# Performance work log

Hardware: AMD Instinct MI355X
Metric: run time of the kernel (lower is better)

The kernel has to match this reference:

```python
import jax, jax.numpy as jnp
import numpy as np

N = 50000      # nodes
E = 800000     # edges (avg degree 16)
IN = 128       # in_channels
OUT = 200      # out_channels


def setup_inputs() -> dict:
    key = jax.random.key(0)
    ks = jax.random.split(key, 12)
    x = jax.random.normal(ks[0], (N, IN), dtype=jnp.float32)
    src = jax.random.randint(ks[1], (E,), 0, N, dtype=jnp.int32)
    off = jax.random.randint(ks[2], (E,), 1, N, dtype=jnp.int32)
    dst = (src + off) % N  # guarantees no self-loops (PyG ChebConv removes them)
    edge_index = jnp.stack([src, dst])
    edge_weight = jax.random.uniform(ks[3], (E,), dtype=jnp.float32) + 0.1
    s = 0.05
    # scale_1 (K=1): one weight; scale_2 (K=2): two; scale_3 (K=3): three. Biases per scale.
    return {
        "x": x,
        "edge_index": edge_index,
        "edge_weight": edge_weight,
        "w1_0": jax.random.normal(ks[4], (IN, OUT), dtype=jnp.float32) * s,
        "b1": jnp.zeros((OUT,), dtype=jnp.float32),
        "w2_0": jax.random.normal(ks[5], (IN, OUT), dtype=jnp.float32) * s,
        "w2_1": jax.random.normal(ks[6], (IN, OUT), dtype=jnp.float32) * s,
        "b2": jnp.zeros((OUT,), dtype=jnp.float32),
        "w3_0": jax.random.normal(ks[7], (IN, OUT), dtype=jnp.float32) * s,
        "w3_1": jax.random.normal(ks[8], (IN, OUT), dtype=jnp.float32) * s,
        "w3_2": jax.random.normal(ks[9], (IN, OUT), dtype=jnp.float32) * s,
        "b3": jnp.zeros((OUT,), dtype=jnp.float32),
    }


def _cheb_norm(edge_index, edge_weight, num_nodes):
    # PyG ChebConv.__norm__ with normalization='sym', lambda_max=2.0:
    # L = I - D^{-1/2} A D^{-1/2}; Lhat = 2L/lambda_max - I = -D^{-1/2} A D^{-1/2}
    # (self-loop weights become exactly 0, so we can drop them)
    row, col = edge_index[0], edge_index[1]
    deg = jax.ops.segment_sum(edge_weight, row, num_segments=num_nodes)
    dis = jnp.where(deg > 0, jax.lax.rsqrt(deg), 0.0)
    return -dis[row] * edge_weight * dis[col]


def _propagate(h, src, dst, norm, num_nodes):
    # out[i] = sum_{(j->i) in E} norm_e * h[j]
    return jax.ops.segment_sum(norm[:, None] * h[src], dst, num_segments=num_nodes)


def reference(x, edge_index, edge_weight, w1_0, b1, w2_0, w2_1, b2, w3_0, w3_1, w3_2, b3):
    num_nodes = x.shape[0]
    src, dst = edge_index[0], edge_index[1]
    norm = _cheb_norm(edge_index, edge_weight, num_nodes)
    # Chebyshev recursion (shared across the three scales; identical math):
    tx0 = x                                              # T_0(L) x
    tx1 = _propagate(tx0, src, dst, norm, num_nodes)     # T_1(L) x = Lhat x
    tx2 = 2.0 * _propagate(tx1, src, dst, norm, num_nodes) - tx0  # T_2(L) x
    s1 = tx0 @ w1_0 + b1
    s2 = tx0 @ w2_0 + tx1 @ w2_1 + b2
    s3 = tx0 @ w3_0 + tx1 @ w3_1 + tx2 @ w3_2 + b3
    return (s1, s2, s3)
```

## Files before the change

kernel.cpp:

```cpp
#include <hip/hip_runtime.h>

#define IN 128
#define OUT 200
#define NT 13
#define MT 64

typedef __bf16 bf16x8 __attribute__((ext_vector_type(8)));
typedef float f32x4 __attribute__((ext_vector_type(4)));
typedef unsigned short ushort;
typedef ushort ushort8 __attribute__((ext_vector_type(8)));
typedef unsigned int uint;

__device__ inline ushort f2bf(float f) {
  uint b = __float_as_uint(f);
  return (ushort)((b + 0x7FFFu + ((b >> 16) & 1u)) >> 16);
}
__device__ inline float bf_lo(uint v) { return __uint_as_float(v << 16); }
__device__ inline float bf_hi(uint v) { return __uint_as_float(v & 0xFFFF0000u); }

__device__ inline size_t pk_idx(int row, int ch) {
  int rt = row >> 4, lr = row & 15, kk = ch >> 5, hi = (ch & 31) >> 3;
  return ((size_t)(rt * 4 + kk) * 64 + hi * 16 + lr) * 8 + (ch & 7);
}

__device__ inline void gload16(const void* g, void* l) {
  __builtin_amdgcn_global_load_lds(
      (const __attribute__((address_space(1))) void*)g,
      (__attribute__((address_space(3))) void*)l, 16, 0, 0);
}


__global__ void k_deg_cnt(const int* __restrict__ src, const int* __restrict__ dst,
                          const float* __restrict__ w, float* __restrict__ deg8,
                          int* __restrict__ cnt8, int E, int N) {
  int e = blockIdx.x * blockDim.x + threadIdx.x;
  if (e >= E) return;
  int copy = blockIdx.x & 7;
  atomicAdd(&deg8[(size_t)copy * N + src[e]], w[e]);
  atomicAdd(&cnt8[(size_t)copy * N + dst[e]], 1);
}

__global__ void k_dis_scan(const float* __restrict__ deg8, const int* __restrict__ cnt8,
                           float* __restrict__ dis, int* __restrict__ pref8,
                           int* __restrict__ offs, int* __restrict__ bsum, int n) {
  __shared__ int s[256];
  int t = threadIdx.x;
  int i = blockIdx.x * 256 + t;
  int v = 0;
  if (i < n) {
    float d = 0.f;
    int run = 0;
#pragma unroll
    for (int c = 0; c < 8; ++c) {
      pref8[(size_t)c * n + i] = run;
      run += cnt8[(size_t)c * n + i];
      d += deg8[(size_t)c * n + i];
    }
    v = run;
    dis[i] = d > 0.f ? rsqrtf(d) : 0.f;
  }
  s[t] = v;
  __syncthreads();
  for (int o = 1; o < 256; o <<= 1) {
    int a = (t >= o) ? s[t - o] : 0;
    __syncthreads();
    s[t] += a;
    __syncthreads();
  }
  if (i < n) offs[i] = s[t] - v;
  if (t == 255) bsum[blockIdx.x] = s[255];
}

__global__ void k_scan_c2(int* __restrict__ offs, const int* __restrict__ bsum,
                          int n, int E) {
  __shared__ int red[256];
  int t = threadIdx.x;
  int partial = 0;
  for (int i = t; i < (int)blockIdx.x; i += 256) partial += bsum[i];
  red[t] = partial;
  __syncthreads();
  for (int o = 128; o > 0; o >>= 1) {
    if (t < o) red[t] += red[t + o];
    __syncthreads();
  }
  int base = red[0];
  int i = blockIdx.x * 256 + t;
  if (i < n) offs[i] += base;
  if (i == 0) offs[n] = E;
}

__global__ void k_fill(const int* __restrict__ src, const int* __restrict__ dst,
                       const float* __restrict__ w, const float* __restrict__ dis,
                       const int* __restrict__ offs, const int* __restrict__ pref8,
                       int* __restrict__ cursor8, int2* __restrict__ csr_rec,
                       int E, int N) {
  int e = blockIdx.x * blockDim.x + threadIdx.x;
  if (e >= E) return;
  int copy = blockIdx.x & 7;
  int sN = src[e], d = dst[e];
  int pos = offs[d] + pref8[(size_t)copy * N + d]
          + atomicAdd(&cursor8[(size_t)copy * N + d], 1);
  float nm = -dis[sN] * w[e] * dis[d];
  csr_rec[pos] = make_int2(sN, __float_as_int(nm));
}


__global__ void k_cast_pack(const float* __restrict__ x, ushort* __restrict__ xb,
                            ushort* __restrict__ xp, int cast_blocks, long totx,
                            const float* __restrict__ w10, const float* __restrict__ w20,
                            const float* __restrict__ w21, const float* __restrict__ w30,
                            const float* __restrict__ w31, const float* __restrict__ w32,
                            ushort* __restrict__ wpack) {
  if (blockIdx.x < (unsigned)cast_blocks) {
    long i = ((long)blockIdx.x * blockDim.x + threadIdx.x) * 8;
    if (i >= totx) return;
    float4 a = *(const float4*)&x[i];
    float4 b = *(const float4*)&x[i + 4];
    ushort8 o;
    o[0] = f2bf(a.x); o[1] = f2bf(a.y); o[2] = f2bf(a.z); o[3] = f2bf(a.w);
    o[4] = f2bf(b.x); o[5] = f2bf(b.y); o[6] = f2bf(b.z); o[7] = f2bf(b.w);
    *(ushort8*)&xb[i] = o;
    int row = (int)(i >> 7), ch = (int)(i & 127);
    *(ushort8*)&xp[pk_idx(row, ch)] = o;
  } else {
    int gid = (blockIdx.x - cast_blocks) * blockDim.x + threadIdx.x;
    int total = 6 * NT * 4 * 64;
    if (gid >= total) return;
    int lane = gid & 63;
    int f = gid >> 6;
    int kk = f & 3;
    int g2 = f >> 2;
    int m = g2 % 6;
    int t = g2 / 6;
    const float* w = (m == 0) ? w10 : (m == 1) ? w20 : (m == 2) ? w21
                   : (m == 3) ? w30 : (m == 4) ? w31 : w32;
    int col = t * 16 + (lane & 15);
    int kbase = kk * 32 + (lane >> 4) * 8;
    ushort8 o;
#pragma unroll
    for (int j = 0; j < 8; ++j)
      o[j] = (col < OUT) ? f2bf(w[(kbase + j) * OUT + col]) : (ushort)0;
    *(ushort8*)&wpack[(size_t)gid * 8] = o;
  }
}


template <int MODE>
__global__ void k_gather(const ushort* __restrict__ h, const ushort* __restrict__ xb,
                         const int2* __restrict__ csr_rec,
                         const int* __restrict__ offs, ushort* __restrict__ out_lin,
                         ushort* __restrict__ out_pk, int n) {
  int node = blockIdx.x * 4 + (threadIdx.x >> 6);
  if (node >= n) return;
  int lane = threadIdx.x & 63;
  int ch0 = lane * 2;
  int s = offs[node], e = offs[node + 1];
  float lo[8], hi[8];
#pragma unroll
  for (int q = 0; q < 8; ++q) { lo[q] = 0.f; hi[q] = 0.f; }
  int p = s;
  for (; p + 7 < e; p += 8) {
    int2 rec[8]; uint v[8];
#pragma unroll
    for (int q = 0; q < 8; ++q) rec[q] = csr_rec[p + q];
#pragma unroll
    for (int q = 0; q < 8; ++q) v[q] = *(const uint*)&h[(size_t)rec[q].x * IN + ch0];
#pragma unroll
    for (int q = 0; q < 8; ++q) {
      float nm = __int_as_float(rec[q].y);
      lo[q] = fmaf(nm, bf_lo(v[q]), lo[q]);
      hi[q] = fmaf(nm, bf_hi(v[q]), hi[q]);
    }
  }
  for (; p + 1 < e; p += 2) {
    int2 r0 = csr_rec[p], r1 = csr_rec[p + 1];
    uint v0 = *(const uint*)&h[(size_t)r0.x * IN + ch0];
    uint v1 = *(const uint*)&h[(size_t)r1.x * IN + ch0];
    float n0 = __int_as_float(r0.y), n1 = __int_as_float(r1.y);
    lo[0] = fmaf(n0, bf_lo(v0), lo[0]); hi[0] = fmaf(n0, bf_hi(v0), hi[0]);
    lo[1] = fmaf(n1, bf_lo(v1), lo[1]); hi[1] = fmaf(n1, bf_hi(v1), hi[1]);
  }
  if (p < e) {
    int2 r0 = csr_rec[p];
    float n0 = __int_as_float(r0.y);
    uint v0 = *(const uint*)&h[(size_t)r0.x * IN + ch0];
    lo[2] = fmaf(n0, bf_lo(v0), lo[2]); hi[2] = fmaf(n0, bf_hi(v0), hi[2]);
  }
  float r0 = ((lo[0] + lo[1]) + (lo[2] + lo[3])) + ((lo[4] + lo[5]) + (lo[6] + lo[7]));
  float r1 = ((hi[0] + hi[1]) + (hi[2] + hi[3])) + ((hi[4] + hi[5]) + (hi[6] + hi[7]));
  if (MODE == 1) {
    uint xv = *(const uint*)&xb[(size_t)node * IN + ch0];
    r0 = 2.f * r0 - bf_lo(xv);
    r1 = 2.f * r1 - bf_hi(xv);
  }
  uint packed = (uint)f2bf(r0) | ((uint)f2bf(r1) << 16);
  if (MODE == 0)
    *(uint*)&out_lin[(size_t)node * IN + ch0] = packed;
  *(uint*)&out_pk[pk_idx(node, ch0)] = packed;
}


__global__ __launch_bounds__(256) void k_gemm_mfma(
    const ushort* __restrict__ xp, const ushort* __restrict__ t1p, const ushort* __restrict__ t2p,
    const ushort* __restrict__ wpack,
    const float* __restrict__ b1v, const float* __restrict__ b2v, const float* __restrict__ b3v,
    float* __restrict__ out, int n) {
  __shared__ ushort bsm[2][24 * 512];
  int lane = threadIdx.x & 63;
  int wave = threadIdx.x >> 6;
  int row0 = blockIdx.x * MT + wave * 16;
  int rt = row0 >> 4;

  bf16x8 a[3][4];
  const ushort* mats[3] = {xp, t1p, t2p};
#pragma unroll
  for (int m = 0; m < 3; ++m) {
#pragma unroll
    for (int kk = 0; kk < 4; ++kk) {
      size_t fi = ((size_t)rt * 4 + kk) * 512 + (size_t)lane * 8;
      a[m][kk] = __builtin_bit_cast(bf16x8, *(const ushort8*)&mats[m][fi]);
    }
  }
#pragma unroll
  for (int m = 0; m < 3; ++m)
#pragma unroll
    for (int kk = 0; kk < 4; ++kk)
      asm volatile("" : "+v"(a[m][kk]));

  long NS = (long)n * OUT;
  float* out1 = out;
  float* out2 = out + NS;
  float* out3 = out + 2 * NS;

  auto stage = [&](int t, int buf) {
    const ushort* src = wpack + (size_t)t * 24 * 512;
#pragma unroll
    for (int j = 0; j < 6; ++j) {
      int c = wave * 6 + j;
      gload16(src + (size_t)c * 512 + (size_t)lane * 8, &bsm[buf][c * 512]);
    }
  };

  stage(0, 0);
  __syncthreads();
  int cur = 0;

  for (int t = 0; t < NT; ++t) {
    if (t + 1 < NT) stage(t + 1, cur ^ 1);

    int col = t * 16 + (lane & 15);
    bool colok = col < OUT;
    int colc = colok ? col : 0;
    float bb1 = colok ? b1v[colc] : 0.f;
    float bb2 = colok ? b2v[colc] : 0.f;
    float bb3 = colok ? b3v[colc] : 0.f;
    f32x4 c1 = {bb1, bb1, bb1, bb1};
    f32x4 c2 = {bb2, bb2, bb2, bb2};
    f32x4 c3 = {bb3, bb3, bb3, bb3};

    const ushort* bb = &bsm[cur][0];
#pragma unroll
    for (int kk = 0; kk < 4; ++kk) {
      bf16x8 b10 = __builtin_bit_cast(bf16x8, *(const ushort8*)&bb[(0 * 4 + kk) * 512 + lane * 8]);
      bf16x8 b20 = __builtin_bit_cast(bf16x8, *(const ushort8*)&bb[(1 * 4 + kk) * 512 + lane * 8]);
      bf16x8 b21 = __builtin_bit_cast(bf16x8, *(const ushort8*)&bb[(2 * 4 + kk) * 512 + lane * 8]);
      bf16x8 b30 = __builtin_bit_cast(bf16x8, *(const ushort8*)&bb[(3 * 4 + kk) * 512 + lane * 8]);
      bf16x8 b31 = __builtin_bit_cast(bf16x8, *(const ushort8*)&bb[(4 * 4 + kk) * 512 + lane * 8]);
      bf16x8 b32 = __builtin_bit_cast(bf16x8, *(const ushort8*)&bb[(5 * 4 + kk) * 512 + lane * 8]);
      c1 = __builtin_amdgcn_mfma_f32_16x16x32_bf16(a[0][kk], b10, c1, 0, 0, 0);
      c2 = __builtin_amdgcn_mfma_f32_16x16x32_bf16(a[0][kk], b20, c2, 0, 0, 0);
      c2 = __builtin_amdgcn_mfma_f32_16x16x32_bf16(a[1][kk], b21, c2, 0, 0, 0);
      c3 = __builtin_amdgcn_mfma_f32_16x16x32_bf16(a[0][kk], b30, c3, 0, 0, 0);
      c3 = __builtin_amdgcn_mfma_f32_16x16x32_bf16(a[1][kk], b31, c3, 0, 0, 0);
      c3 = __builtin_amdgcn_mfma_f32_16x16x32_bf16(a[2][kk], b32, c3, 0, 0, 0);
    }

    if (colok) {
      int rbase = row0 + (lane >> 4) * 4;
#pragma unroll
      for (int r = 0; r < 4; ++r) {
        int ra = rbase + r;
        if (ra < n) {
          out1[(long)ra * OUT + col] = c1[r];
          out2[(long)ra * OUT + col] = c2[r];
          out3[(long)ra * OUT + col] = c3[r];
        }
      }
    }

    __syncthreads();
    cur ^= 1;
  }
}


extern "C" void kernel_launch(void* const* d_in, const int* in_sizes, int n_in,
                              void* d_out, int out_size, void* d_ws, size_t ws_size,
                              hipStream_t stream) {
  const float* x   = (const float*)d_in[0];
  const int*   ei  = (const int*)d_in[1];
  const float* ew  = (const float*)d_in[2];
  const float* w10 = (const float*)d_in[3];
  const float* b1  = (const float*)d_in[4];
  const float* w20 = (const float*)d_in[5];
  const float* w21 = (const float*)d_in[6];
  const float* b2  = (const float*)d_in[7];
  const float* w30 = (const float*)d_in[8];
  const float* w31 = (const float*)d_in[9];
  const float* w32 = (const float*)d_in[10];
  const float* b3  = (const float*)d_in[11];
  float* out = (float*)d_out;

  int N = in_sizes[0] / IN;
  int E = in_sizes[2];
  const int* src = ei;
  const int* dst = ei + E;

  int mtiles = (N + MT - 1) / MT;
  size_t prow = (size_t)mtiles * MT;
  size_t pksz = prow * IN * 2;

  char* ws = (char*)d_ws;
  size_t off = 0;
  auto alloc = [&](size_t bytes) {
    void* p = ws + off;
    off = (off + bytes + 15) & ~(size_t)15;
    return p;
  };
  float* deg8     = (float*)alloc((size_t)8 * N * 4);
  int*   cnt8     = (int*)alloc((size_t)8 * N * 4);
  int*   cursor8  = (int*)alloc((size_t)8 * N * 4);
  int*   pref8    = (int*)alloc((size_t)8 * N * 4);
  float* dis      = (float*)alloc((size_t)N * 4);
  int*   offs     = (int*)alloc(((size_t)N + 1) * 4);
  int2*  csr_rec  = (int2*)alloc((size_t)E * 8);
  int*   bsum     = (int*)alloc(256 * 4);
  ushort* xb      = (ushort*)alloc((size_t)N * IN * 2);
  ushort* tx1b    = (ushort*)alloc((size_t)N * IN * 2);
  ushort* xp      = (ushort*)alloc(pksz);
  ushort* t1p     = (ushort*)alloc(pksz);
  ushort* t2p     = (ushort*)alloc(pksz);
  ushort* wpack   = (ushort*)alloc((size_t)6 * NT * 4 * 64 * 8 * 2);

  hipMemsetAsync(deg8, 0, (size_t)24 * N * 4, stream);

  const int tb = 256;
  int ge = (E + tb - 1) / tb;
  int nb = (N + 255) / 256;

  long totx = (long)N * IN;
  int cast_blocks = (int)((totx / 8 + tb - 1) / tb);
  int wp_blocks = (6 * NT * 4 * 64 + tb - 1) / tb;

  k_deg_cnt<<<ge, tb, 0, stream>>>(src, dst, ew, deg8, cnt8, E, N);
  k_dis_scan<<<nb, 256, 0, stream>>>(deg8, cnt8, dis, pref8, offs, bsum, N);
  k_scan_c2<<<nb, 256, 0, stream>>>(offs, bsum, N, E);
  k_fill<<<ge, tb, 0, stream>>>(src, dst, ew, dis, offs, pref8, cursor8, csr_rec, E, N);
  k_cast_pack<<<cast_blocks + wp_blocks, tb, 0, stream>>>(
      x, xb, xp, cast_blocks, totx, w10, w20, w21, w30, w31, w32, wpack);

  int gblk = (N + 3) / 4;
  k_gather<0><<<gblk, 256, 0, stream>>>(xb, xb, csr_rec, offs, tx1b, t1p, N);
  k_gather<1><<<gblk, 256, 0, stream>>>(tx1b, xb, csr_rec, offs, nullptr, t2p, N);

  k_gemm_mfma<<<mtiles, 256, 0, stream>>>(xp, t1p, t2p, wpack, b1, b2, b3, out, N);
}
```

Measured before the change: 267.5 us.

## Build CSR with LDS-privatized histograms over node ranges and edge slices

Replaces the global-atomic degree/count histogram and the fill cursor with block-local LDS atomics. Each block owns one node range and one edge slice, so the memset and the global atomics go away. Only 64 blocks are launched, and each block scans its whole edge slice once per range, so src/dst are read 8 times. That risks underusing the GPU and adding memory traffic on the many-CU MI355X.

```diff
diff --git a/kernel.cpp b/kernel.cpp
--- a/kernel.cpp
+++ b/kernel.cpp
@@ -4,6 +4,9 @@
 #define OUT 200
 #define NT 13
 #define MT 64
+#define RANGES 8
+#define REPLICAS 8
+#define RBMAX 6272
 
 typedef __bf16 bf16x8 __attribute__((ext_vector_type(8)));
 typedef float f32x4 __attribute__((ext_vector_type(4)));
@@ -30,17 +33,33 @@
 }
 
 
-__global__ void k_deg_cnt(const int* __restrict__ src, const int* __restrict__ dst,
-                          const float* __restrict__ w, float* __restrict__ deg8,
-                          int* __restrict__ cnt8, int E, int N) {
-  int e = blockIdx.x * blockDim.x + threadIdx.x;
-  if (e >= E) return;
-  int copy = blockIdx.x & 7;
-  atomicAdd(&deg8[(size_t)copy * N + src[e]], w[e]);
-  atomicAdd(&cnt8[(size_t)copy * N + dst[e]], 1);
-}
-
-__global__ void k_dis_scan(const float* __restrict__ deg8, const int* __restrict__ cnt8,
+__global__ __launch_bounds__(256) void k_hist(
+    const int* __restrict__ src, const int* __restrict__ dst,
+    const float* __restrict__ w, float* __restrict__ deg_part,
+    int* __restrict__ cnt_part, int E, int N, int RB, int SL) {
+  __shared__ float degL[RBMAX];
+  __shared__ int cntL[RBMAX];
+  int range = blockIdx.x / REPLICAS;
+  int rep = blockIdx.x % REPLICAS;
+  int base = range * RB;
+  int lim = min(N - base, RB);
+  for (int i = threadIdx.x; i < RB; i += 256) { degL[i] = 0.f; cntL[i] = 0; }
+  __syncthreads();
+  int e0 = rep * SL, e1 = min(E, e0 + SL);
+  for (int e = e0 + (int)threadIdx.x; e < e1; e += 256) {
+    int s = src[e], d = dst[e];
+    int sl = s - base, dl = d - base;
+    if ((unsigned)sl < (unsigned)lim) atomicAdd(&degL[sl], w[e]);
+    if ((unsigned)dl < (unsigned)lim) atomicAdd(&cntL[dl], 1);
+  }
+  __syncthreads();
+  for (int i = threadIdx.x; i < lim; i += 256) {
+    deg_part[(size_t)rep * N + base + i] = degL[i];
+    cnt_part[(size_t)rep * N + base + i] = cntL[i];
+  }
+}
+
+__global__ void k_dis_scan(const float* __restrict__ deg_part, const int* __restrict__ cnt_part,
                            float* __restrict__ dis, int* __restrict__ pref8,
                            int* __restrict__ offs, int* __restrict__ bsum, int n) {
   __shared__ int s[256];
@@ -51,10 +70,10 @@
     float d = 0.f;
     int run = 0;
 #pragma unroll
-    for (int c = 0; c < 8; ++c) {
+    for (int c = 0; c < REPLICAS; ++c) {
       pref8[(size_t)c * n + i] = run;
-      run += cnt8[(size_t)c * n + i];
-      d += deg8[(size_t)c * n + i];
+      run += cnt_part[(size_t)c * n + i];
+      d += deg_part[(size_t)c * n + i];
     }
     v = run;
     dis[i] = d > 0.f ? rsqrtf(d) : 0.f;
@@ -89,19 +108,30 @@
   if (i == 0) offs[n] = E;
 }
 
-__global__ void k_fill(const int* __restrict__ src, const int* __restrict__ dst,
-                       const float* __restrict__ w, const float* __restrict__ dis,
-                       const int* __restrict__ offs, const int* __restrict__ pref8,
-                       int* __restrict__ cursor8, int2* __restrict__ csr_rec,
-                       int E, int N) {
-  int e = blockIdx.x * blockDim.x + threadIdx.x;
-  if (e >= E) return;
-  int copy = blockIdx.x & 7;
-  int sN = src[e], d = dst[e];
-  int pos = offs[d] + pref8[(size_t)copy * N + d]
-          + atomicAdd(&cursor8[(size_t)copy * N + d], 1);
-  float nm = -dis[sN] * w[e] * dis[d];
-  csr_rec[pos] = make_int2(sN, __float_as_int(nm));
+__global__ __launch_bounds__(256) void k_fill(
+    const int* __restrict__ src, const int* __restrict__ dst,
+    const float* __restrict__ w, const float* __restrict__ dis,
+    const int* __restrict__ offs, const int* __restrict__ pref8,
+    int2* __restrict__ csr_rec, int E, int N, int RB, int SL) {
+  __shared__ int curL[RBMAX];
+  int range = blockIdx.x / REPLICAS;
+  int rep = blockIdx.x % REPLICAS;
+  int base = range * RB;
+  int lim = min(N - base, RB);
+  for (int i = threadIdx.x; i < RB; i += 256) curL[i] = 0;
+  __syncthreads();
+  int e0 = rep * SL, e1 = min(E, e0 + SL);
+  for (int e = e0 + (int)threadIdx.x; e < e1; e += 256) {
+    int d = dst[e];
+    int dl = d - base;
+    if ((unsigned)dl < (unsigned)lim) {
+      int s = src[e];
+      int r = atomicAdd(&curL[dl], 1);
+      int pos = offs[d] + pref8[(size_t)rep * N + d] + r;
+      float nm = -dis[s] * w[e] * dis[d];
+      csr_rec[pos] = make_int2(s, __float_as_int(nm));
+    }
+  }
 }
 
 
@@ -320,6 +350,9 @@
   size_t prow = (size_t)mtiles * MT;
   size_t pksz = prow * IN * 2;
 
+  int RB = (N + RANGES - 1) / RANGES;
+  int SL = (E + REPLICAS - 1) / REPLICAS;
+
   char* ws = (char*)d_ws;
   size_t off = 0;
   auto alloc = [&](size_t bytes) {
@@ -327,10 +360,9 @@
     off = (off + bytes + 15) & ~(size_t)15;
     return p;
   };
-  float* deg8     = (float*)alloc((size_t)8 * N * 4);
-  int*   cnt8     = (int*)alloc((size_t)8 * N * 4);
-  int*   cursor8  = (int*)alloc((size_t)8 * N * 4);
-  int*   pref8    = (int*)alloc((size_t)8 * N * 4);
+  float* deg_part = (float*)alloc((size_t)REPLICAS * N * 4);
+  int*   cnt_part = (int*)alloc((size_t)REPLICAS * N * 4);
+  int*   pref8    = (int*)alloc((size_t)REPLICAS * N * 4);
   float* dis      = (float*)alloc((size_t)N * 4);
   int*   offs     = (int*)alloc(((size_t)N + 1) * 4);
   int2*  csr_rec  = (int2*)alloc((size_t)E * 8);
@@ -342,20 +374,17 @@
   ushort* t2p     = (ushort*)alloc(pksz);
   ushort* wpack   = (ushort*)alloc((size_t)6 * NT * 4 * 64 * 8 * 2);
 
-  hipMemsetAsync(deg8, 0, (size_t)24 * N * 4, stream);
-
   const int tb = 256;
-  int ge = (E + tb - 1) / tb;
   int nb = (N + 255) / 256;
 
   long totx = (long)N * IN;
   int cast_blocks = (int)((totx / 8 + tb - 1) / tb);
   int wp_blocks = (6 * NT * 4 * 64 + tb - 1) / tb;
 
-  k_deg_cnt<<<ge, tb, 0, stream>>>(src, dst, ew, deg8, cnt8, E, N);
-  k_dis_scan<<<nb, 256, 0, stream>>>(deg8, cnt8, dis, pref8, offs, bsum, N);
+  k_hist<<<RANGES * REPLICAS, 256, 0, stream>>>(src, dst, ew, deg_part, cnt_part, E, N, RB, SL);
+  k_dis_scan<<<nb, 256, 0, stream>>>(deg_part, cnt_part, dis, pref8, offs, bsum, N);
   k_scan_c2<<<nb, 256, 0, stream>>>(offs, bsum, N, E);
-  k_fill<<<ge, tb, 0, stream>>>(src, dst, ew, dis, offs, pref8, cursor8, csr_rec, E, N);
+  k_fill<<<RANGES * REPLICAS, 256, 0, stream>>>(src, dst, ew, dis, offs, pref8, csr_rec, E, N, RB, SL);
   k_cast_pack<<<cast_blocks + wp_blocks, tb, 0, stream>>>(
       x, xb, xp, cast_blocks, totx, w10, w20, w21, w30, w31, w32, wpack);
 
```

Result: slower. 596.8 us (+123.1%).
